# Performance work log

Hardware: AMD Instinct MI355X
Metric: run time of the kernel (lower is better)

## Reference

```python
import jax, jax.numpy as jnp
import numpy as np

LN_EPS = 1e-5


def setup_inputs() -> dict:
    key = jax.random.key(0)
    b, n_f, n_i, d = 8, 16, 128, 256
    x = jax.random.normal(key, (b, n_f, n_i, d), dtype=jnp.float32)
    gamma = jnp.ones((d,), dtype=jnp.float32)
    beta = jnp.zeros((d,), dtype=jnp.float32)
    return {"x": x, "gamma": gamma, "beta": beta}


def reference(x, gamma, beta):
    # x: (b, n_f, n_i, d). Dropout layers are identity in eval mode.
    n_f = x.shape[1]
    # sinusoidal frame positional scalar: sin(cumsum(1)/10000) -> sin((1..n_f)/1e4)
    pos = jnp.sin(jnp.arange(1, n_f + 1, dtype=jnp.float32) / 10000.0)  # (n_f,)
    # scores[b, i, j, m, c] = pos[i] * (x[b, j, m, c] + pos[j])
    scores = pos[None, :, None, None, None] * (
        x[:, None, :, :, :] + pos[None, None, :, None, None]
    )  # (b, n_f, n_f, n_i, d)
    atten = jax.nn.softmax(scores, axis=2)  # softmax over source frame j
    # v[b, i, m, c] = sum_j x[b, j, m, c] * atten[b, i, j, m, c]
    v = jnp.sum(x[:, None, :, :, :] * atten, axis=2)  # (b, n_f, n_i, d)
    y = x + v
    # LayerNorm over last dim d
    mu = jnp.mean(y, axis=-1, keepdims=True)
    var = jnp.mean(jnp.square(y - mu), axis=-1, keepdims=True)
    out = (y - mu) * jax.lax.rsqrt(var + LN_EPS) * gamma + beta
    return out
```

## Files before the change

### kernel.cpp

```cpp
#include <hip/hip_runtime.h>
#include <math.h>

#define B_  8
#define NF  16
#define NI  128
#define D_  256
#define LN_EPS 1e-5f

__global__ __launch_bounds__(256, 1)
void temporal_attn_ln(const float* __restrict__ x,
                      const float* __restrict__ gamma,
                      const float* __restrict__ beta,
                      float* __restrict__ out) {
    const int wave = threadIdx.x >> 6;
    const int lane = threadIdx.x & 63;
    const int bm   = (blockIdx.x << 2) + wave;
    const int b    = bm >> 7;
    const int m    = bm & (NI - 1);
    const int c0   = lane << 2;

    const size_t fs   = (size_t)NI * D_;
    const size_t base = ((size_t)b * NF * NI + (size_t)m) * D_ + (size_t)c0;

    float4 xv[NF];
#pragma unroll
    for (int j = 0; j < NF; ++j)
        xv[j] = *reinterpret_cast<const float4*>(x + base + (size_t)j * fs);

    const float4 g4  = *reinterpret_cast<const float4*>(gamma + c0);
    const float4 be4 = *reinterpret_cast<const float4*>(beta  + c0);

    float pos[NF];
#pragma unroll
    for (int j = 0; j < NF; ++j) pos[j] = __sinf((float)(j + 1) * 1e-4f);

    float4 X0 = make_float4(0.f, 0.f, 0.f, 0.f);
    float4 X1 = X0, X2 = X0, T1 = X0, T2 = X0;
#pragma unroll
    for (int j = 0; j < NF; ++j) {
        const float4 xj = xv[j];
        const float  pj = pos[j];
        float4 t, xt;
        t.x = xj.x + pj;  t.y = xj.y + pj;  t.z = xj.z + pj;  t.w = xj.w + pj;
        xt.x = xj.x * t.x; xt.y = xj.y * t.y; xt.z = xj.z * t.z; xt.w = xj.w * t.w;
        X0.x += xj.x; X0.y += xj.y; X0.z += xj.z; X0.w += xj.w;
        X1.x += xt.x; X1.y += xt.y; X1.z += xt.z; X1.w += xt.w;
        X2.x = fmaf(xt.x, t.x, X2.x); X2.y = fmaf(xt.y, t.y, X2.y);
        X2.z = fmaf(xt.z, t.z, X2.z); X2.w = fmaf(xt.w, t.w, X2.w);
        T1.x += t.x; T1.y += t.y; T1.z += t.z; T1.w += t.w;
        T2.x = fmaf(t.x, t.x, T2.x); T2.y = fmaf(t.y, t.y, T2.y);
        T2.z = fmaf(t.z, t.z, T2.z); T2.w = fmaf(t.w, t.w, T2.w);
    }

#pragma unroll
    for (int i = 0; i < NF; i += 2) {
        float4 yy[2];
        float  s[2], s2[2];
#pragma unroll
        for (int k = 0; k < 2; ++k) {
            const float pi = pos[i + k];
            const float h  = 0.5f * pi * pi;
            float4 num, den, r, v, y;
            num.x = fmaf(h, X2.x, fmaf(pi, X1.x, X0.x));
            num.y = fmaf(h, X2.y, fmaf(pi, X1.y, X0.y));
            num.z = fmaf(h, X2.z, fmaf(pi, X1.z, X0.z));
            num.w = fmaf(h, X2.w, fmaf(pi, X1.w, X0.w));
            den.x = fmaf(h, T2.x, fmaf(pi, T1.x, (float)NF));
            den.y = fmaf(h, T2.y, fmaf(pi, T1.y, (float)NF));
            den.z = fmaf(h, T2.z, fmaf(pi, T1.z, (float)NF));
            den.w = fmaf(h, T2.w, fmaf(pi, T1.w, (float)NF));
            r.x = __builtin_amdgcn_rcpf(den.x);
            r.y = __builtin_amdgcn_rcpf(den.y);
            r.z = __builtin_amdgcn_rcpf(den.z);
            r.w = __builtin_amdgcn_rcpf(den.w);
            r.x *= fmaf(-den.x, r.x, 2.0f);
            r.y *= fmaf(-den.y, r.y, 2.0f);
            r.z *= fmaf(-den.z, r.z, 2.0f);
            r.w *= fmaf(-den.w, r.w, 2.0f);
            v.x = num.x * r.x; v.y = num.y * r.y;
            v.z = num.z * r.z; v.w = num.w * r.w;
            const float4 xi = xv[i + k];
            y.x = xi.x + v.x; y.y = xi.y + v.y;
            y.z = xi.z + v.z; y.w = xi.w + v.w;
            yy[k] = y;
            s[k]  = (y.x + y.y) + (y.z + y.w);
            s2[k] = fmaf(y.x, y.x, fmaf(y.y, y.y, fmaf(y.z, y.z, y.w * y.w)));
        }
#pragma unroll
        for (int off = 32; off; off >>= 1) {
            s[0]  += __shfl_xor(s[0],  off, 64);
            s2[0] += __shfl_xor(s2[0], off, 64);
            s[1]  += __shfl_xor(s[1],  off, 64);
            s2[1] += __shfl_xor(s2[1], off, 64);
        }
#pragma unroll
        for (int k = 0; k < 2; ++k) {
            const float mu  = s[k] * (1.0f / D_);
            const float var = fmaf(s2[k], 1.0f / D_, -mu * mu);
            const float inv = rsqrtf(var + LN_EPS);
            const float4 y  = yy[k];
            float4 o;
            o.x = fmaf((y.x - mu) * inv, g4.x, be4.x);
            o.y = fmaf((y.y - mu) * inv, g4.y, be4.y);
            o.z = fmaf((y.z - mu) * inv, g4.z, be4.z);
            o.w = fmaf((y.w - mu) * inv, g4.w, be4.w);
            *reinterpret_cast<float4*>(out + base + (size_t)(i + k) * fs) = o;
        }
    }
}

extern "C" void kernel_launch(void* const* d_in, const int* in_sizes, int n_in,
                              void* d_out, int out_size, void* d_ws, size_t ws_size,
                              hipStream_t stream) {
    const float* x     = (const float*)d_in[0];
    const float* gamma = (const float*)d_in[1];
    const float* beta  = (const float*)d_in[2];
    float* out         = (float*)d_out;

    dim3 grid((B_ * NI) / 4);
    dim3 block(256);
    temporal_attn_ln<<<grid, block, 0, stream>>>(x, gamma, beta, out);
}
```

Measured before the change: 19.14 us.

## Split output frames across two waves and batch LayerNorm reductions via transpose-shuffle

Each (b,m) column is now handled by two waves, each producing 8 of the 16 output frames, which doubles the grid and raises occupancy via launch_bounds(256,2). Both waves still load all 16 input frames, so x reads double. The per-frame LayerNorm sum reductions are batched with a butterfly transpose that reduces 8 values in fewer shuffles, and the results are then broadcast with readlane. The sine is replaced by a Taylor approximation, exact enough for these tiny arguments, and T1 is derived from X0 plus the sum of positions.

```diff
diff --git a/kernel.cpp b/kernel.cpp
--- a/kernel.cpp
+++ b/kernel.cpp
@@ -7,14 +7,22 @@
 #define D_  256
 #define LN_EPS 1e-5f
 
-__global__ __launch_bounds__(256, 1)
+__device__ __forceinline__ float rl(float v, int l) {
+    return __int_as_float(__builtin_amdgcn_readlane(__float_as_int(v), l));
+}
+__device__ __forceinline__ float sin_taylor(float a) {
+    return a * fmaf(a * a, -(1.0f / 6.0f), 1.0f);
+}
+
+__global__ __launch_bounds__(256, 2)
 void temporal_attn_ln(const float* __restrict__ x,
                       const float* __restrict__ gamma,
                       const float* __restrict__ beta,
                       float* __restrict__ out) {
-    const int wave = threadIdx.x >> 6;
+    const int gw   = (blockIdx.x << 2) + (threadIdx.x >> 6);
+    const int bm   = gw >> 1;
+    const int half = gw & 1;
     const int lane = threadIdx.x & 63;
-    const int bm   = (blockIdx.x << 2) + wave;
     const int b    = bm >> 7;
     const int m    = bm & (NI - 1);
     const int c0   = lane << 2;
@@ -31,81 +39,99 @@
     const float4 be4 = *reinterpret_cast<const float4*>(beta  + c0);
 
     float pos[NF];
+    float P1 = 0.0f;
 #pragma unroll
-    for (int j = 0; j < NF; ++j) pos[j] = __sinf((float)(j + 1) * 1e-4f);
+    for (int j = 0; j < NF; ++j) {
+        pos[j] = sin_taylor((float)(j + 1) * 1e-4f);
+        P1 += pos[j];
+    }
 
     float4 X0 = make_float4(0.f, 0.f, 0.f, 0.f);
-    float4 X1 = X0, X2 = X0, T1 = X0, T2 = X0;
+    float4 X1 = X0, X2 = X0, T2 = X0;
 #pragma unroll
     for (int j = 0; j < NF; ++j) {
         const float4 xj = xv[j];
         const float  pj = pos[j];
         float4 t, xt;
-        t.x = xj.x + pj;  t.y = xj.y + pj;  t.z = xj.z + pj;  t.w = xj.w + pj;
+        t.x = xj.x + pj;   t.y = xj.y + pj;   t.z = xj.z + pj;   t.w = xj.w + pj;
         xt.x = xj.x * t.x; xt.y = xj.y * t.y; xt.z = xj.z * t.z; xt.w = xj.w * t.w;
         X0.x += xj.x; X0.y += xj.y; X0.z += xj.z; X0.w += xj.w;
         X1.x += xt.x; X1.y += xt.y; X1.z += xt.z; X1.w += xt.w;
         X2.x = fmaf(xt.x, t.x, X2.x); X2.y = fmaf(xt.y, t.y, X2.y);
         X2.z = fmaf(xt.z, t.z, X2.z); X2.w = fmaf(xt.w, t.w, X2.w);
-        T1.x += t.x; T1.y += t.y; T1.z += t.z; T1.w += t.w;
-        T2.x = fmaf(t.x, t.x, T2.x); T2.y = fmaf(t.y, t.y, T2.y);
-        T2.z = fmaf(t.z, t.z, T2.z); T2.w = fmaf(t.w, t.w, T2.w);
+        T2.x = fmaf(t.x, t.x, T2.x);  T2.y = fmaf(t.y, t.y, T2.y);
+        T2.z = fmaf(t.z, t.z, T2.z);  T2.w = fmaf(t.w, t.w, T2.w);
+    }
+    float4 T1;
+    T1.x = X0.x + P1; T1.y = X0.y + P1; T1.z = X0.z + P1; T1.w = X0.w + P1;
+
+    float4 yy[8];
+    float  s[8], q[8];
+#pragma unroll
+    for (int di = 0; di < 8; ++di) {
+        const float a  = (float)((half << 3) + di + 1) * 1e-4f;
+        const float pi = sin_taylor(a);
+        const float h  = 0.5f * pi * pi;
+        float4 num, den, r, y;
+        num.x = fmaf(h, X2.x, fmaf(pi, X1.x, X0.x));
+        num.y = fmaf(h, X2.y, fmaf(pi, X1.y, X0.y));
+        num.z = fmaf(h, X2.z, fmaf(pi, X1.z, X0.z));
+        num.w = fmaf(h, X2.w, fmaf(pi, X1.w, X0.w));
+        den.x = fmaf(h, T2.x, fmaf(pi, T1.x, (float)NF));
+        den.y = fmaf(h, T2.y, fmaf(pi, T1.y, (float)NF));
+        den.z = fmaf(h, T2.z, fmaf(pi, T1.z, (float)NF));
+        den.w = fmaf(h, T2.w, fmaf(pi, T1.w, (float)NF));
+        r.x = __builtin_amdgcn_rcpf(den.x);  r.x *= fmaf(-den.x, r.x, 2.0f);
+        r.y = __builtin_amdgcn_rcpf(den.y);  r.y *= fmaf(-den.y, r.y, 2.0f);
+        r.z = __builtin_amdgcn_rcpf(den.z);  r.z *= fmaf(-den.z, r.z, 2.0f);
+        r.w = __builtin_amdgcn_rcpf(den.w);  r.w *= fmaf(-den.w, r.w, 2.0f);
+        const float4 xi = xv[(half << 3) + di];
+        y.x = fmaf(num.x, r.x, xi.x); y.y = fmaf(num.y, r.y, xi.y);
+        y.z = fmaf(num.z, r.z, xi.z); y.w = fmaf(num.w, r.w, xi.w);
+        yy[di] = y;
+        s[di]  = (y.x + y.y) + (y.z + y.w);
+        q[di]  = fmaf(y.x, y.x, fmaf(y.y, y.y, fmaf(y.z, y.z, y.w * y.w)));
     }
 
+    const bool hi5 = (lane & 32) != 0;
+    const bool hi4 = (lane & 16) != 0;
+    const bool hi3 = (lane & 8)  != 0;
+    float sa[4], qa[4];
 #pragma unroll
-    for (int i = 0; i < NF; i += 2) {
-        float4 yy[2];
-        float  s[2], s2[2];
+    for (int k = 0; k < 4; ++k) {
+        const float ss = __shfl_xor(hi5 ? s[k] : s[k + 4], 32, 64);
+        const float qq = __shfl_xor(hi5 ? q[k] : q[k + 4], 32, 64);
+        sa[k] = (hi5 ? s[k + 4] : s[k]) + ss;
+        qa[k] = (hi5 ? q[k + 4] : q[k]) + qq;
+    }
+    float sb[2], qb[2];
 #pragma unroll
-        for (int k = 0; k < 2; ++k) {
-            const float pi = pos[i + k];
-            const float h  = 0.5f * pi * pi;
-            float4 num, den, r, v, y;
-            num.x = fmaf(h, X2.x, fmaf(pi, X1.x, X0.x));
-            num.y = fmaf(h, X2.y, fmaf(pi, X1.y, X0.y));
-            num.z = fmaf(h, X2.z, fmaf(pi, X1.z, X0.z));
-            num.w = fmaf(h, X2.w, fmaf(pi, X1.w, X0.w));
-            den.x = fmaf(h, T2.x, fmaf(pi, T1.x, (float)NF));
-            den.y = fmaf(h, T2.y, fmaf(pi, T1.y, (float)NF));
-            den.z = fmaf(h, T2.z, fmaf(pi, T1.z, (float)NF));
-            den.w = fmaf(h, T2.w, fmaf(pi, T1.w, (float)NF));
-            r.x = __builtin_amdgcn_rcpf(den.x);
-            r.y = __builtin_amdgcn_rcpf(den.y);
-            r.z = __builtin_amdgcn_rcpf(den.z);
-            r.w = __builtin_amdgcn_rcpf(den.w);
-            r.x *= fmaf(-den.x, r.x, 2.0f);
-            r.y *= fmaf(-den.y, r.y, 2.0f);
-            r.z *= fmaf(-den.z, r.z, 2.0f);
-            r.w *= fmaf(-den.w, r.w, 2.0f);
-            v.x = num.x * r.x; v.y = num.y * r.y;
-            v.z = num.z * r.z; v.w = num.w * r.w;
-            const float4 xi = xv[i + k];
-            y.x = xi.x + v.x; y.y = xi.y + v.y;
-            y.z = xi.z + v.z; y.w = xi.w + v.w;
-            yy[k] = y;
-            s[k]  = (y.x + y.y) + (y.z + y.w);
-            s2[k] = fmaf(y.x, y.x, fmaf(y.y, y.y, fmaf(y.z, y.z, y.w * y.w)));
-        }
+    for (int k = 0; k < 2; ++k) {
+        const float ss = __shfl_xor(hi4 ? sa[k] : sa[k + 2], 16, 64);
+        const float qq = __shfl_xor(hi4 ? qa[k] : qa[k + 2], 16, 64);
+        sb[k] = (hi4 ? sa[k + 2] : sa[k]) + ss;
+        qb[k] = (hi4 ? qa[k + 2] : qa[k]) + qq;
+    }
+    float S = (hi3 ? sb[1] : sb[0]) + __shfl_xor(hi3 ? sb[0] : sb[1], 8, 64);
+    float Q = (hi3 ? qb[1] : qb[0]) + __shfl_xor(hi3 ? qb[0] : qb[1], 8, 64);
+    S += __shfl_xor(S, 4, 64);  Q += __shfl_xor(Q, 4, 64);
+    S += __shfl_xor(S, 2, 64);  Q += __shfl_xor(Q, 2, 64);
+    S += __shfl_xor(S, 1, 64);  Q += __shfl_xor(Q, 1, 64);
+    const float mu_o  = S * (1.0f / D_);
+    const float var_o = fmaf(Q, 1.0f / D_, -mu_o * mu_o);
+    const float inv_o = rsqrtf(var_o + LN_EPS);
+
 #pragma unroll
-        for (int off = 32; off; off >>= 1) {
-            s[0]  += __shfl_xor(s[0],  off, 64);
-            s2[0] += __shfl_xor(s2[0], off, 64);
-            s[1]  += __shfl_xor(s[1],  off, 64);
-            s2[1] += __shfl_xor(s2[1], off, 64);
-        }
-#pragma unroll
-        for (int k = 0; k < 2; ++k) {
-            const float mu  = s[k] * (1.0f / D_);
-            const float var = fmaf(s2[k], 1.0f / D_, -mu * mu);
-            const float inv = rsqrtf(var + LN_EPS);
-            const float4 y  = yy[k];
-            float4 o;
-            o.x = fmaf((y.x - mu) * inv, g4.x, be4.x);
-            o.y = fmaf((y.y - mu) * inv, g4.y, be4.y);
-            o.z = fmaf((y.z - mu) * inv, g4.z, be4.z);
-            o.w = fmaf((y.w - mu) * inv, g4.w, be4.w);
-            *reinterpret_cast<float4*>(out + base + (size_t)(i + k) * fs) = o;
-        }
+    for (int di = 0; di < 8; ++di) {
+        const float mu  = rl(mu_o,  di << 3);
+        const float inv = rl(inv_o, di << 3);
+        const float4 y  = yy[di];
+        float4 o;
+        o.x = fmaf((y.x - mu) * inv, g4.x, be4.x);
+        o.y = fmaf((y.y - mu) * inv, g4.y, be4.y);
+        o.z = fmaf((y.z - mu) * inv, g4.z, be4.z);
+        o.w = fmaf((y.w - mu) * inv, g4.w, be4.w);
+        *reinterpret_cast<float4*>(out + base + (size_t)((half << 3) + di) * fs) = o;
     }
 }
 
@@ -117,7 +143,7 @@
     const float* beta  = (const float*)d_in[2];
     float* out         = (float*)d_out;
 
-    dim3 grid((B_ * NI) / 4);
+    dim3 grid((B_ * NI * 2) / 4);
     dim3 block(256);
     temporal_attn_ln<<<grid, block, 0, stream>>>(x, gamma, beta, out);
 }
```

Result: slower. 19.60 us (+2.4%).
